# Kernel optimization log

Measured on AMD Instinct MI355X. Metric: run time of the kernel, lower is better.

The kernel has to match this reference:

```python
import jax, jax.numpy as jnp
import numpy as np

D_LOW = 32
LAGS = [1, 2, 4, 8]
# Upper-triangular pair indices (offset=1), matching torch.triu_indices(d_low, d_low, 1)
IDX_I, IDX_J = np.triu_indices(D_LOW, k=1)
IDX_I = jnp.asarray(IDX_I)
IDX_J = jnp.asarray(IDX_J)
EPS = 1e-6


def setup_inputs() -> dict:
    key = jax.random.key(0)
    ks = jax.random.split(key, 7)
    b, n, d_model = 4, 4096, 1024
    d_plucker = D_LOW * (D_LOW - 1) // 2  # 496
    s = lambda fan_in: 1.0 / np.sqrt(fan_in)
    return {
        "x": jax.random.normal(ks[0], (b, n, d_model), dtype=jnp.float32),
        "W_red": jax.random.normal(ks[1], (d_model, D_LOW), dtype=jnp.float32) * s(d_model),
        "b_red": jax.random.normal(ks[2], (D_LOW,), dtype=jnp.float32) * s(d_model),
        "W_exp": jax.random.normal(ks[3], (d_plucker, d_model), dtype=jnp.float32) * s(d_plucker),
        "b_exp": jax.random.normal(ks[4], (d_model,), dtype=jnp.float32) * s(d_plucker),
        "W_gate": jax.random.normal(ks[5], (2 * d_model, d_model), dtype=jnp.float32) * s(2 * d_model),
        "b_gate": jax.random.normal(ks[6], (d_model,), dtype=jnp.float32) * s(2 * d_model),
    }


def reference(x, W_red, b_red, W_exp, b_exp, W_gate, b_gate):
    b, n, _ = x.shape
    d_plucker = D_LOW * (D_LOW - 1) // 2
    z = x @ W_red + b_red  # [b, n, d_low]
    plucker_total = jnp.zeros((b, n, d_plucker), dtype=x.dtype)
    counts = jnp.zeros((b, n, 1), dtype=x.dtype)
    for lag in LAGS:
        if lag <= 0 or lag >= n:
            continue
        z_curr = z[:, lag:, :]   # [b, n-lag, d_low]
        z_past = z[:, :-lag, :]  # [b, n-lag, d_low]
        # Antisymmetric Plucker coordinates over upper-triangular index pairs
        p = (z_curr[:, :, IDX_I] * z_past[:, :, IDX_J]
             - z_curr[:, :, IDX_J] * z_past[:, :, IDX_I])  # [b, n-lag, d_plucker]
        norm = jnp.linalg.norm(p, axis=-1, keepdims=True)
        p = p / jnp.maximum(norm, EPS)
        plucker_total = plucker_total.at[:, lag:, :].add(p)
        counts = counts.at[:, lag:, :].add(1.0)
    counts = jnp.maximum(counts, 1.0)
    plucker_avg = plucker_total / counts
    g_avg = plucker_avg @ W_exp + b_exp  # [b, n, d_model]
    concat = jnp.concatenate([x, g_avg], axis=-1)  # [b, n, 2*d_model]
    gate = jax.nn.sigmoid(concat @ W_gate + b_gate)
    return gate * x + (1.0 - gate) * g_avg
```

## Files before the change

### kernel.cpp

```cpp
#include <hip/hip_runtime.h>
#include <hip/hip_bf16.h>
#include <math.h>

#define B_DIM   4
#define N_DIM   4096
#define D_MODEL 1024
#define D_LOW   32
#define NPAIR   496
#define NROWS   (B_DIM * N_DIM)
#define KPAD3   512
#define LDA2    1536

typedef __bf16 bf16;
typedef __bf16 bf16x8 __attribute__((ext_vector_type(8)));
typedef __bf16 bf16x4 __attribute__((ext_vector_type(4)));
typedef float  f32x4  __attribute__((ext_vector_type(4)));

#define GLOAD_LDS16(g, l) __builtin_amdgcn_global_load_lds( \
    (__attribute__((address_space(1))) void*)(g),           \
    (__attribute__((address_space(3))) void*)(l), 16, 0, 0)

__global__ __launch_bounds__(256) void transpose3(const float* __restrict__ Wg,
                                                  const float* __restrict__ We,
                                                  const float* __restrict__ Wr,
                                                  const float* __restrict__ be,
                                                  bf16* __restrict__ BcT,
                                                  bf16* __restrict__ WgbT,
                                                  bf16* __restrict__ WeT,
                                                  bf16* __restrict__ WrT,
                                                  bf16* __restrict__ WeB) {
    __shared__ float tile[32][36];
    const int z = blockIdx.z;
    const int t = threadIdx.x;
    if (z == 3) {
        const int flat = blockIdx.y * 32 + blockIdx.x;
        if (flat >= 544) return;
        if (flat < 32) {
            const int kb = flat * 32;
            {
                int k = t >> 3, c4 = (t & 7) * 4;
                float4 v = *reinterpret_cast<const float4*>(&Wr[(size_t)(kb + k) * 32 + c4]);
                tile[k][c4 + 0] = v.x; tile[k][c4 + 1] = v.y;
                tile[k][c4 + 2] = v.z; tile[k][c4 + 3] = v.w;
            }
            __syncthreads();
            {
                int c = t >> 3, kq = (t & 7) * 4;
                bf16x4 o = { (bf16)tile[kq + 0][c], (bf16)tile[kq + 1][c],
                             (bf16)tile[kq + 2][c], (bf16)tile[kq + 3][c] };
                *reinterpret_cast<bf16x4*>(&WrT[(size_t)c * 1024 + kb + kq]) = o;
            }
        } else {
            size_t o = ((size_t)(flat - 32) * 256 + t) * 4;
            int row = (int)(o >> 10), col = (int)(o & 1023);
            float4 v = {0.f, 0.f, 0.f, 0.f};
            if (row < NPAIR)       v = *reinterpret_cast<const float4*>(&We[(size_t)row * 1024 + col]);
            else if (row == NPAIR) v = *reinterpret_cast<const float4*>(&be[col]);
            bf16x4 b = { (bf16)v.x, (bf16)v.y, (bf16)v.z, (bf16)v.w };
            *reinterpret_cast<bf16x4*>(&WeB[o]) = b;
        }
        return;
    }
    const float* src = (z == 0) ? Wg : (z == 1) ? (Wg + (size_t)1024 * 1024) : We;
    bf16* dst  = (z == 0) ? BcT : (z == 1) ? WgbT : WeT;
    const int Kpad = (z == 0) ? 1536 : (z == 1) ? 1024 : 512;
    const int Ksrc = (z == 2) ? NPAIR : 1024;
    const int kb = blockIdx.x * 32;
    if (kb >= Kpad) return;
    const int nb = blockIdx.y * 32;
    int li = t * 4;
    int kl = li >> 5, nl = li & 31;
    float4 v = {0.f, 0.f, 0.f, 0.f};
    if (kb + kl < Ksrc)
        v = *reinterpret_cast<const float4*>(&src[(size_t)(kb + kl) * 1024 + nb + nl]);
    tile[kl][nl + 0] = v.x; tile[kl][nl + 1] = v.y;
    tile[kl][nl + 2] = v.z; tile[kl][nl + 3] = v.w;
    __syncthreads();
    int nl2 = li >> 5, kl2 = li & 31;
    bf16x4 o = { (bf16)tile[kl2 + 0][nl2], (bf16)tile[kl2 + 1][nl2],
                 (bf16)tile[kl2 + 2][nl2], (bf16)tile[kl2 + 3][nl2] };
    *reinterpret_cast<bf16x4*>(&dst[(size_t)(nb + nl2) * Kpad + kb + kl2]) = o;
}

__global__ __launch_bounds__(256) void wcomb_wave(const bf16* __restrict__ WgbT,
                                                  const bf16* __restrict__ WeB,
                                                  bf16* __restrict__ BcT) {
    const int t    = threadIdx.x;
    const int wv   = t >> 6, lane = t & 63;
    const int l15  = lane & 15, lhi = lane >> 4;
    const int kk0  = blockIdx.x * 16;
    const int n0   = blockIdx.y * 64 + wv * 16;
    f32x4 acc = (f32x4){0.f, 0.f, 0.f, 0.f};
#pragma unroll 8
    for (int kb = 0; kb < 1024; kb += 32) {
        const bf16x8 af = *reinterpret_cast<const bf16x8*>(
            &WgbT[(size_t)(n0 + l15) * 1024 + kb + lhi * 8]);
        const bf16x8 bf = *reinterpret_cast<const bf16x8*>(
            &WeB[(size_t)(kk0 + l15) * 1024 + kb + lhi * 8]);
        acc = __builtin_amdgcn_mfma_f32_16x16x32_bf16(af, bf, acc, 0, 0, 0);
    }
#pragma unroll
    for (int r = 0; r < 4; ++r) {
        const int n = n0 + lhi * 4 + r;
        BcT[(size_t)n * 1536 + 1024 + kk0 + l15] = (bf16)acc[r];
    }
}

__global__ __launch_bounds__(256) void k1_mfma(const float* __restrict__ x,
                                               const bf16* __restrict__ WrT,
                                               bf16* __restrict__ a2,
                                               float* __restrict__ zpart) {
    const int t    = threadIdx.x;
    const int wv   = t >> 6, lane = t & 63;
    const int l15  = lane & 15, lhi = lane >> 4;
    const int kc   = blockIdx.x;
    const int mt   = blockIdx.y;
    const int row  = mt * 64 + wv * 16 + l15;
    const int kb   = kc * 256;

    f32x4 accz[2] = { (f32x4){0.f,0.f,0.f,0.f}, (f32x4){0.f,0.f,0.f,0.f} };

#pragma unroll
    for (int ks = 0; ks < 8; ++ks) {
        const int k0 = kb + ks * 32 + lhi * 8;
        const float4 u0 = *reinterpret_cast<const float4*>(&x[(size_t)row * 1024 + k0]);
        const float4 u1 = *reinterpret_cast<const float4*>(&x[(size_t)row * 1024 + k0 + 4]);
        bf16x8 af = { (bf16)u0.x, (bf16)u0.y, (bf16)u0.z, (bf16)u0.w,
                      (bf16)u1.x, (bf16)u1.y, (bf16)u1.z, (bf16)u1.w };
        *reinterpret_cast<bf16x8*>(&a2[(size_t)row * LDA2 + k0]) = af;
        const bf16x8 b0 = *reinterpret_cast<const bf16x8*>(
            &WrT[(size_t)l15 * 1024 + kb + ks * 32 + lhi * 8]);
        const bf16x8 b1 = *reinterpret_cast<const bf16x8*>(
            &WrT[(size_t)(16 + l15) * 1024 + kb + ks * 32 + lhi * 8]);
        accz[0] = __builtin_amdgcn_mfma_f32_16x16x32_bf16(af, b0, accz[0], 0, 0, 0);
        accz[1] = __builtin_amdgcn_mfma_f32_16x16x32_bf16(af, b1, accz[1], 0, 0, 0);
    }
#pragma unroll
    for (int cg = 0; cg < 2; ++cg)
#pragma unroll
        for (int r = 0; r < 4; ++r) {
            const int rout = mt * 64 + wv * 16 + lhi * 4 + r;
            zpart[((size_t)kc * NROWS + rout) * 32 + cg * 16 + l15] = accz[cg][r];
        }
}

__global__ __launch_bounds__(256) void k2_plucker(const float* __restrict__ zpart,
                                                  const float* __restrict__ br,
                                                  bf16* __restrict__ a2) {
    const int wv   = threadIdx.x >> 6;
    const int lane = threadIdx.x & 63;
    const int row  = blockIdx.x * 4 + wv;
    const int t    = row & (N_DIM - 1);
    const int c    = lane & 31;
    const float bias = br[c];

    float zc = bias;
#pragma unroll
    for (int p = 0; p < 4; ++p)
        zc += zpart[((size_t)p * NROWS + row) * 32 + c];

    float zp[4];
    float red[9];
    red[0] = zc * zc;
#pragma unroll
    for (int li = 0; li < 4; ++li) {
        const int lag = 1 << li;
        float v = 0.f;
        if (t >= lag) {
            v = bias;
#pragma unroll
            for (int p = 0; p < 4; ++p)
                v += zpart[((size_t)p * NROWS + (row - lag)) * 32 + c];
        }
        zp[li] = v;
        red[1 + li] = zc * zp[li];
        red[5 + li] = zp[li] * zp[li];
    }
#pragma unroll
    for (int m = 1; m < 32; m <<= 1) {
#pragma unroll
        for (int i = 0; i < 9; ++i) red[i] += __shfl_xor(red[i], m);
    }
    float cnt = 0.f;
#pragma unroll
    for (int li = 0; li < 4; ++li) cnt += (t >= (1 << li)) ? 1.f : 0.f;
    const float inv = 1.f / fmaxf(cnt, 1.f);

    float w = 0.f;
#pragma unroll
    for (int li = 0; li < 4; ++li) {
        float n2 = fmaxf(red[0] * red[5 + li] - red[1 + li] * red[1 + li], 0.f);
        float nr = sqrtf(n2);
        float s  = (t >= (1 << li)) ? inv / fmaxf(nr, 1e-6f) : 0.f;
        w += s * zp[li];
    }

#pragma unroll
    for (int u = 0; u < 8; ++u) {
        const int k = u * 64 + lane;
        float v = 0.f;
        if (k < NPAIR) {
            int kk = k, i = 0;
            while (kk >= 31 - i) { kk -= 31 - i; ++i; }
            const int j = i + 1 + kk;
            float zci = __shfl(zc, i), zcj = __shfl(zc, j);
            float wi  = __shfl(w, i),  wj  = __shfl(w, j);
            v = zci * wj - zcj * wi;
        }
        a2[(size_t)row * LDA2 + 1024 + k] = (bf16)v;
    }
}

__global__ __launch_bounds__(256, 2) void gemmfu(const bf16* __restrict__ A,
                                                 const bf16* __restrict__ Bt,
                                                 const bf16* __restrict__ WeT,
                                                 const float* __restrict__ bg,
                                                 const float* __restrict__ be,
                                                 float* __restrict__ out) {
    extern __shared__ char lds[];
    const int t    = threadIdx.x;
    const int w    = t >> 6, lane = t & 63;
    const int wr   = w >> 1, wc = w & 1;
    const int l15  = lane & 15, lhi = lane >> 4;

    const int fid = blockIdx.x;
    const int xcd = fid & 7, loc = fid >> 3;
    const int mb  = (xcd * 16 + (loc >> 3)) * 128;
    const int nb  = (loc & 7) * 128;

    char* const ldsA = lds;
    char* const ldsB = lds + 32768;

    const int srow1 = t >> 3;
    const int scol1 = ((t & 7) ^ (srow1 & 7)) * 8;
    const size_t aOff1 = (size_t)(mb + srow1) * LDA2 + scol1;
    const size_t bOff1 = (size_t)(nb + srow1) * 1536 + scol1;
#define STAGE1(d, kb) do { \
    _Pragma("unroll") for (int q = 0; q < 4; ++q) \
        GLOAD_LDS16(A + aOff1 + (size_t)(q * 32) * LDA2 + (kb), \
                    ldsA + (d) * 16384 + q * 4096 + t * 16); \
    _Pragma("unroll") for (int q = 0; q < 4; ++q) \
        GLOAD_LDS16(Bt + bOff1 + (size_t)(q * 32) * 1536 + (kb), \
                    ldsB + (d) * 16384 + q * 4096 + t * 16); } while (0)

    const int srow2 = t >> 2;
    const int scol2 = ((t & 3) ^ ((srow2 >> 1) & 3)) * 8;
    const size_t aOff2 = (size_t)(mb + srow2) * LDA2 + 1024 + scol2;
    const size_t bOff2 = (size_t)(nb + srow2) * 1536 + 1024 + scol2;
    const size_t wOff2 = (size_t)(nb + srow2) * 512 + scol2;
#define STAGE2(d, kb) do { \
    GLOAD_LDS16(A + aOff2 + (kb),                        ldsA + (d) * 16384 + t * 16); \
    GLOAD_LDS16(A + aOff2 + (size_t)64 * LDA2 + (kb),    ldsA + (d) * 16384 + 4096 + t * 16); \
    GLOAD_LDS16(Bt + bOff2 + (kb),                       ldsB + (d) * 16384 + t * 16); \
    GLOAD_LDS16(Bt + bOff2 + (size_t)64 * 1536 + (kb),   ldsB + (d) * 16384 + 4096 + t * 16); \
    GLOAD_LDS16(WeT + wOff2 + (kb),                      ldsB + (d) * 16384 + 8192 + t * 16); \
    GLOAD_LDS16(WeT + wOff2 + (size_t)64 * 512 + (kb),   ldsB + (d) * 16384 + 8192 + 4096 + t * 16); } while (0)

    const int swx1 = (l15 & 7) << 4;
    const int swr2 = ((l15 >> 1) & 3) << 4;

    f32x4 acc[4][4], acc2[4][4];
#pragma unroll
    for (int i = 0; i < 4; ++i)
#pragma unroll
        for (int j = 0; j < 4; ++j) {
            acc[i][j]  = (f32x4){0.f, 0.f, 0.f, 0.f};
            acc2[i][j] = (f32x4){0.f, 0.f, 0.f, 0.f};
        }
    bf16x8 afr[4][2], bfr[4][2];

    STAGE1(0, 0);

    for (int kt = 0; kt < 16; ++kt) {
        const int d = kt & 1;
        asm volatile("s_barrier" ::: "memory");
        if (kt < 15) {
            STAGE1(d ^ 1, (kt + 1) * 64);
            asm volatile("s_waitcnt vmcnt(8)" ::: "memory");
        } else {
            STAGE2(d ^ 1, 0);
            asm volatile("s_waitcnt vmcnt(6)" ::: "memory");
        }
        asm volatile("s_barrier" ::: "memory");

        const char* Ab = ldsA + d * 16384;
        const char* Bb = ldsB + d * 16384;
#pragma unroll
        for (int mf = 0; mf < 4; ++mf)
#pragma unroll
            for (int ks = 0; ks < 2; ++ks) {
                int lin = (wr * 64 + mf * 16 + l15) * 128 + ks * 64 + lhi * 16;
                afr[mf][ks] = *reinterpret_cast<const bf16x8*>(Ab + (lin ^ swx1));
            }
#pragma unroll
        for (int nf = 0; nf < 4; ++nf)
#pragma unroll
            for (int ks = 0; ks < 2; ++ks) {
                int lin = (wc * 64 + nf * 16 + l15) * 128 + ks * 64 + lhi * 16;
                bfr[nf][ks] = *reinterpret_cast<const bf16x8*>(Bb + (lin ^ swx1));
            }
        __builtin_amdgcn_s_setprio(1);
#pragma unroll
        for (int mf = 0; mf < 4; ++mf)
#pragma unroll
            for (int nf = 0; nf < 4; ++nf)
#pragma unroll
                for (int ks = 0; ks < 2; ++ks)
                    acc[mf][nf] = __builtin_amdgcn_mfma_f32_16x16x32_bf16(
                        afr[mf][ks], bfr[nf][ks], acc[mf][nf], 0, 0, 0);
        __builtin_amdgcn_s_setprio(0);
    }

    for (int ft = 0; ft < 16; ++ft) {
        const int d = ft & 1;
        asm volatile("s_barrier" ::: "memory");
        if (ft < 15) {
            STAGE2(d ^ 1, (ft + 1) * 32);
            asm volatile("s_waitcnt vmcnt(6)" ::: "memory");
        } else {
            asm volatile("s_waitcnt vmcnt(0)" ::: "memory");
        }
        asm volatile("s_barrier" ::: "memory");

        const char* Ab = ldsA + d * 16384;
        const char* Bb = ldsB + d * 16384;
        bf16x8 a2f[4], bcf[4], wef[4];
#pragma unroll
        for (int mf = 0; mf < 4; ++mf) {
            int lin = (wr * 64 + mf * 16 + l15) * 64 + ((lhi * 16) ^ swr2);
            a2f[mf] = *reinterpret_cast<const bf16x8*>(Ab + lin);
        }
#pragma unroll
        for (int nf = 0; nf < 4; ++nf) {
            int lin = (wc * 64 + nf * 16 + l15) * 64 + ((lhi * 16) ^ swr2);
            bcf[nf] = *reinterpret_cast<const bf16x8*>(Bb + lin);
            wef[nf] = *reinterpret_cast<const bf16x8*>(Bb + 8192 + lin);
        }
        __builtin_amdgcn_s_setprio(1);
#pragma unroll
        for (int mf = 0; mf < 4; ++mf)
#pragma unroll
            for (int nf = 0; nf < 4; ++nf) {
                acc[mf][nf]  = __builtin_amdgcn_mfma_f32_16x16x32_bf16(
                    a2f[mf], bcf[nf], acc[mf][nf], 0, 0, 0);
                acc2[mf][nf] = __builtin_amdgcn_mfma_f32_16x16x32_bf16(
                    a2f[mf], wef[nf], acc2[mf][nf], 0, 0, 0);
            }
        __builtin_amdgcn_s_setprio(0);
    }

#pragma unroll
    for (int mf = 0; mf < 4; ++mf) {
#pragma unroll
        for (int nf = 0; nf < 4; ++nf) {
            const int col = nb + wc * 64 + nf * 16 + l15;
            const float bgate = bg[col] + (float)Bt[(size_t)col * 1536 + 1024 + NPAIR];
            const float bexp  = be[col];
#pragma unroll
            for (int r = 0; r < 4; ++r) {
                const int row = mb + wr * 64 + mf * 16 + lhi * 4 + r;
                const float s    = acc[mf][nf][r] + bgate;
                const float gate = 1.f / (1.f + expf(-s));
                const float g    = acc2[mf][nf][r] + bexp;
                const float xv   = (float)A[(size_t)row * LDA2 + col];
                out[(size_t)row * D_MODEL + col] = gate * xv + (1.f - gate) * g;
            }
        }
    }
}

extern "C" void kernel_launch(void* const* d_in, const int* in_sizes, int n_in,
                              void* d_out, int out_size, void* d_ws, size_t ws_size,
                              hipStream_t stream) {
    const float* x  = (const float*)d_in[0];
    const float* Wr = (const float*)d_in[1];
    const float* br = (const float*)d_in[2];
    const float* We = (const float*)d_in[3];
    const float* be = (const float*)d_in[4];
    const float* Wg = (const float*)d_in[5];
    const float* bg = (const float*)d_in[6];
    float* out = (float*)d_out;

    char* ws = (char*)d_ws;
    float* zpart = (float*)(ws);
    bf16*  A2    = (bf16*)(ws + (32u << 20));
    bf16*  WeT   = (bf16*)(ws + (80u << 20));
    bf16*  BcT   = (bf16*)(ws + (81u << 20));
    bf16*  WgbT  = (bf16*)(ws + (84u << 20));
    bf16*  WeB   = (bf16*)(ws + (86u << 20));
    bf16*  WrT   = (bf16*)(ws + (88u << 20));

    (void)hipFuncSetAttribute(reinterpret_cast<const void*>(&gemmfu),
                              hipFuncAttributeMaxDynamicSharedMemorySize, 65536);

    transpose3<<<dim3(32, 32, 4), 256, 0, stream>>>(Wg, We, Wr, be,
                                                    BcT, WgbT, WeT, WrT, WeB);
    wcomb_wave<<<dim3(32, 16), 256, 0, stream>>>(WgbT, WeB, BcT);
    k1_mfma<<<dim3(4, 256), 256, 0, stream>>>(x, WrT, A2, zpart);
    k2_plucker<<<NROWS / 4, 256, 0, stream>>>(zpart, br, A2);
    gemmfu<<<1024, 256, 65536, stream>>>(A2, BcT, WeT, bg, be, out);
}
```

Baseline: 149.0 us.

## Drop LDS double buffering in fused GEMM to fit four blocks per CU

Replaces the double-buffered LDS staging in the fused gate/expand GEMM with a single buffer, halving dynamic shared memory to 32 KB. Each k-step now loads and then waits for all loads before computing. Launch bounds are raised to four blocks per CU so the whole grid fits in one wave, relying on occupancy to hide latency. The trade is no intra-block overlap of loads and MFMA, plus a tighter register budget for the two large accumulator sets, which may cause spills.

```diff
diff --git a/kernel.cpp b/kernel.cpp
--- a/kernel.cpp
+++ b/kernel.cpp
@@ -211,7 +211,7 @@
     }
 }
 
-__global__ __launch_bounds__(256, 2) void gemmfu(const bf16* __restrict__ A,
+__global__ __launch_bounds__(256, 4) void gemmfu(const bf16* __restrict__ A,
                                                  const bf16* __restrict__ Bt,
                                                  const bf16* __restrict__ WeT,
                                                  const float* __restrict__ bg,
@@ -229,32 +229,32 @@
     const int nb  = (loc & 7) * 128;
 
     char* const ldsA = lds;
-    char* const ldsB = lds + 32768;
+    char* const ldsB = lds + 16384;
 
     const int srow1 = t >> 3;
     const int scol1 = ((t & 7) ^ (srow1 & 7)) * 8;
     const size_t aOff1 = (size_t)(mb + srow1) * LDA2 + scol1;
     const size_t bOff1 = (size_t)(nb + srow1) * 1536 + scol1;
-#define STAGE1(d, kb) do { \
+#define STAGE1(kb) do { \
     _Pragma("unroll") for (int q = 0; q < 4; ++q) \
         GLOAD_LDS16(A + aOff1 + (size_t)(q * 32) * LDA2 + (kb), \
-                    ldsA + (d) * 16384 + q * 4096 + t * 16); \
+                    ldsA + q * 4096 + t * 16); \
     _Pragma("unroll") for (int q = 0; q < 4; ++q) \
         GLOAD_LDS16(Bt + bOff1 + (size_t)(q * 32) * 1536 + (kb), \
-                    ldsB + (d) * 16384 + q * 4096 + t * 16); } while (0)
+                    ldsB + q * 4096 + t * 16); } while (0)
 
     const int srow2 = t >> 2;
     const int scol2 = ((t & 3) ^ ((srow2 >> 1) & 3)) * 8;
     const size_t aOff2 = (size_t)(mb + srow2) * LDA2 + 1024 + scol2;
     const size_t bOff2 = (size_t)(nb + srow2) * 1536 + 1024 + scol2;
     const size_t wOff2 = (size_t)(nb + srow2) * 512 + scol2;
-#define STAGE2(d, kb) do { \
-    GLOAD_LDS16(A + aOff2 + (kb),                        ldsA + (d) * 16384 + t * 16); \
-    GLOAD_LDS16(A + aOff2 + (size_t)64 * LDA2 + (kb),    ldsA + (d) * 16384 + 4096 + t * 16); \
-    GLOAD_LDS16(Bt + bOff2 + (kb),                       ldsB + (d) * 16384 + t * 16); \
-    GLOAD_LDS16(Bt + bOff2 + (size_t)64 * 1536 + (kb),   ldsB + (d) * 16384 + 4096 + t * 16); \
-    GLOAD_LDS16(WeT + wOff2 + (kb),                      ldsB + (d) * 16384 + 8192 + t * 16); \
-    GLOAD_LDS16(WeT + wOff2 + (size_t)64 * 512 + (kb),   ldsB + (d) * 16384 + 8192 + 4096 + t * 16); } while (0)
+#define STAGE2(kb) do { \
+    GLOAD_LDS16(A + aOff2 + (kb),                        ldsA + t * 16); \
+    GLOAD_LDS16(A + aOff2 + (size_t)64 * LDA2 + (kb),    ldsA + 4096 + t * 16); \
+    GLOAD_LDS16(Bt + bOff2 + (kb),                       ldsB + t * 16); \
+    GLOAD_LDS16(Bt + bOff2 + (size_t)64 * 1536 + (kb),   ldsB + 4096 + t * 16); \
+    GLOAD_LDS16(WeT + wOff2 + (kb),                      ldsB + 8192 + t * 16); \
+    GLOAD_LDS16(WeT + wOff2 + (size_t)64 * 512 + (kb),   ldsB + 8192 + 4096 + t * 16); } while (0)
 
     const int swx1 = (l15 & 7) << 4;
     const int swr2 = ((l15 >> 1) & 3) << 4;
@@ -269,35 +269,25 @@
         }
     bf16x8 afr[4][2], bfr[4][2];
 
-    STAGE1(0, 0);
-
     for (int kt = 0; kt < 16; ++kt) {
-        const int d = kt & 1;
         asm volatile("s_barrier" ::: "memory");
-        if (kt < 15) {
-            STAGE1(d ^ 1, (kt + 1) * 64);
-            asm volatile("s_waitcnt vmcnt(8)" ::: "memory");
-        } else {
-            STAGE2(d ^ 1, 0);
-            asm volatile("s_waitcnt vmcnt(6)" ::: "memory");
-        }
+        STAGE1(kt * 64);
+        asm volatile("s_waitcnt vmcnt(0)" ::: "memory");
         asm volatile("s_barrier" ::: "memory");
 
-        const char* Ab = ldsA + d * 16384;
-        const char* Bb = ldsB + d * 16384;
 #pragma unroll
         for (int mf = 0; mf < 4; ++mf)
 #pragma unroll
             for (int ks = 0; ks < 2; ++ks) {
                 int lin = (wr * 64 + mf * 16 + l15) * 128 + ks * 64 + lhi * 16;
-                afr[mf][ks] = *reinterpret_cast<const bf16x8*>(Ab + (lin ^ swx1));
+                afr[mf][ks] = *reinterpret_cast<const bf16x8*>(ldsA + (lin ^ swx1));
             }
 #pragma unroll
         for (int nf = 0; nf < 4; ++nf)
 #pragma unroll
             for (int ks = 0; ks < 2; ++ks) {
                 int lin = (wc * 64 + nf * 16 + l15) * 128 + ks * 64 + lhi * 16;
-                bfr[nf][ks] = *reinterpret_cast<const bf16x8*>(Bb + (lin ^ swx1));
+                bfr[nf][ks] = *reinterpret_cast<const bf16x8*>(ldsB + (lin ^ swx1));
             }
         __builtin_amdgcn_s_setprio(1);
 #pragma unroll
@@ -312,29 +302,22 @@
     }
 
     for (int ft = 0; ft < 16; ++ft) {
-        const int d = ft & 1;
         asm volatile("s_barrier" ::: "memory");
-        if (ft < 15) {
-            STAGE2(d ^ 1, (ft + 1) * 32);
-            asm volatile("s_waitcnt vmcnt(6)" ::: "memory");
-        } else {
-            asm volatile("s_waitcnt vmcnt(0)" ::: "memory");
-        }
+        STAGE2(ft * 32);
+        asm volatile("s_waitcnt vmcnt(0)" ::: "memory");
         asm volatile("s_barrier" ::: "memory");
 
-        const char* Ab = ldsA + d * 16384;
-        const char* Bb = ldsB + d * 16384;
         bf16x8 a2f[4], bcf[4], wef[4];
 #pragma unroll
         for (int mf = 0; mf < 4; ++mf) {
             int lin = (wr * 64 + mf * 16 + l15) * 64 + ((lhi * 16) ^ swr2);
-            a2f[mf] = *reinterpret_cast<const bf16x8*>(Ab + lin);
+            a2f[mf] = *reinterpret_cast<const bf16x8*>(ldsA + lin);
         }
 #pragma unroll
         for (int nf = 0; nf < 4; ++nf) {
             int lin = (wc * 64 + nf * 16 + l15) * 64 + ((lhi * 16) ^ swr2);
-            bcf[nf] = *reinterpret_cast<const bf16x8*>(Bb + lin);
-            wef[nf] = *reinterpret_cast<const bf16x8*>(Bb + 8192 + lin);
+            bcf[nf] = *reinterpret_cast<const bf16x8*>(ldsB + lin);
+            wef[nf] = *reinterpret_cast<const bf16x8*>(ldsB + 8192 + lin);
         }
         __builtin_amdgcn_s_setprio(1);
 #pragma unroll
@@ -391,12 +374,12 @@
     bf16*  WrT   = (bf16*)(ws + (88u << 20));
 
     (void)hipFuncSetAttribute(reinterpret_cast<const void*>(&gemmfu),
-                              hipFuncAttributeMaxDynamicSharedMemorySize, 65536);
+                              hipFuncAttributeMaxDynamicSharedMemorySize, 32768);
 
     transpose3<<<dim3(32, 32, 4), 256, 0, stream>>>(Wg, We, Wr, be,
                                                     BcT, WgbT, WeT, WrT, WeB);
     wcomb_wave<<<dim3(32, 16), 256, 0, stream>>>(WgbT, WeB, BcT);
     k1_mfma<<<dim3(4, 256), 256, 0, stream>>>(x, WrT, A2, zpart);
     k2_plucker<<<NROWS / 4, 256, 0, stream>>>(zpart, br, A2);
-    gemmfu<<<1024, 256, 65536, stream>>>(A2, BcT, WeT, bg, be, out);
-}
+    gemmfu<<<1024, 256, 32768, stream>>>(A2, BcT, WeT, bg, be, out);
+}
```

New measurement: 564.3 us. 279% more time.
